# Kernel optimization log

Hardware: AMD Instinct MI355X
Metric: run time of the kernel (lower is better)

The kernel has to match this reference:

```python
import jax, jax.numpy as jnp
import numpy as np

H, W = 80, 80
LOWPASS = 0.3   # 3DGS low-pass filter added to 2D covariance diagonal
NEAR = 0.2      # near-plane cull depth


def quat_to_rot(q):
    # q: [N,4] (w,x,y,z) -> [N,3,3]
    w, x, y, z = q[..., 0], q[..., 1], q[..., 2], q[..., 3]
    return jnp.stack([
        jnp.stack([1 - 2 * (y * y + z * z), 2 * (x * y - w * z), 2 * (x * z + w * y)], -1),
        jnp.stack([2 * (x * y + w * z), 1 - 2 * (x * x + z * z), 2 * (y * z - w * x)], -1),
        jnp.stack([2 * (x * z - w * y), 2 * (y * z + w * x), 1 - 2 * (x * x + y * y)], -1),
    ], -2)


def setup_inputs() -> dict:
    key = jax.random.key(0)
    k1, k2 = jax.random.split(key)
    vsize = 1.25
    def mids(lo, hi, lim):
        g = np.arange(lo, hi + 1e-6, vsize)
        return ((g[:-1] + g[1:]) / 2.0)[:lim]
    xy = mids(-20.0, 20.0, 200)   # 32 midpoints
    zz = mids(-4.0, 4.0, 16)      # 6 midpoints
    X, Y, Z = np.meshgrid(xy, xy, zz, indexing='ij')
    pc_xyz = jnp.asarray(np.stack([X, Y, Z], -1).reshape(-1, 3), jnp.float32)  # [6144,3]
    N = pc_xyz.shape[0]
    B, NC, C = 1, 6, 32
    vox_features = jax.random.normal(k1, (B, N, C), jnp.float32)
    density = jax.random.normal(k2, (B, N), jnp.float32)
    scales = jnp.full((N, 1), float(np.log(vsize)), jnp.float32)
    rots = jnp.concatenate([jnp.ones((N, 1)), jnp.zeros((N, 3))], -1).astype(jnp.float32)
    # 6 surround cameras at origin, yaw = k*60deg; cam axes: x=right, y=up-ish, z=forward
    yaws = np.arange(NC) * (2 * np.pi / NC)
    f = np.stack([np.cos(yaws), np.sin(yaws), np.zeros(NC)], -1)
    r = np.stack([np.sin(yaws), -np.cos(yaws), np.zeros(NC)], -1)
    u = np.cross(f, r)
    Rw2c = np.stack([r, u, f], 1)  # rows are camera axes -> world2cam rotation [NC,3,3]
    cam_rot = jnp.asarray(Rw2c[None], jnp.float32)          # [B,NC,3,3]
    cam_trans = jnp.zeros((B, NC, 3), jnp.float32)          # [B,NC,3]
    cam_intr = jnp.asarray(np.tile(np.array([45.0, 45.0, W / 2.0, H / 2.0], np.float32), (B, NC, 1)))
    return dict(vox_features=vox_features, density=density, cam_rot=cam_rot,
                cam_trans=cam_trans, cam_intr=cam_intr, pc_xyz=pc_xyz,
                scales=scales, rots=rots)


def _render_one(Rcw, t, intr, pc_xyz, Mcov, opacity, feats):
    # Rcw [3,3], t [3], intr [4]; Mcov [N,3,3] = R*diag(s); opacity [N]; feats [N,C]
    fx, fy, cx, cy = intr[0], intr[1], intr[2], intr[3]
    cam = pc_xyz @ Rcw.T + t                    # [N,3] camera-frame means
    tz = jnp.maximum(cam[:, 2], 1e-6)
    valid = (cam[:, 2] > NEAR).astype(pc_xyz.dtype)
    u = fx * cam[:, 0] / tz + cx
    v = fy * cam[:, 1] / tz + cy
    z0 = jnp.zeros_like(tz)
    J = jnp.stack([jnp.stack([fx / tz, z0, -fx * cam[:, 0] / tz ** 2], -1),
                   jnp.stack([z0, fy / tz, -fy * cam[:, 1] / tz ** 2], -1)], -2)  # [N,2,3]
    A = jnp.einsum('nij,jk->nik', J, Rcw)       # J @ W  [N,2,3]
    Bm = jnp.einsum('nij,njk->nik', A, Mcov)    # [N,2,3]
    cov = jnp.einsum('nij,nkj->nik', Bm, Bm)    # 2D covariance [N,2,2]
    a = cov[:, 0, 0] + LOWPASS
    b = cov[:, 0, 1]
    c = cov[:, 1, 1] + LOWPASS
    det = a * c - b * b
    ia, ib, ic = c / det, -b / det, a / det
    # depth-sort (invalid gaussians pushed to the back)
    order = jnp.argsort(tz + (1.0 - valid) * 1e6)
    u, v, ia, ib, ic = u[order], v[order], ia[order], ib[order], ic[order]
    op_s, feat_s, valid_s = opacity[order], feats[order], valid[order]
    px = jnp.arange(W, dtype=pc_xyz.dtype)
    py = jnp.arange(H, dtype=pc_xyz.dtype)
    dx = px[None, None, :] - u[:, None, None]   # [N,1,W] -> broadcast [N,H,W]
    dy = py[None, :, None] - v[:, None, None]   # [N,H,1]
    power = (-0.5 * (ia[:, None, None] * dx * dx + ic[:, None, None] * dy * dy)
             - ib[:, None, None] * dx * dy)
    g = jnp.exp(jnp.minimum(power, 0.0))
    alpha = jnp.clip(op_s[:, None, None] * g, 0.0, 0.99) * valid_s[:, None, None]
    Tcum = jnp.cumprod(1.0 - alpha, axis=0)
    Texc = jnp.concatenate([jnp.ones((1, H, W), alpha.dtype), Tcum[:-1]], 0)  # exclusive transmittance
    return jnp.einsum('nhw,nc->chw', Texc * alpha, feat_s)


def reference(vox_features, density, cam_rot, cam_trans, cam_intr, pc_xyz, scales, rots):
    Bsz, N, C = vox_features.shape
    Rg = quat_to_rot(rots)                      # [N,3,3]
    s = jnp.exp(scales)                         # [N,1] isotropic scale
    Mcov = Rg * s[:, :, None]                   # R @ diag(s,s,s)
    outs = []
    for b in range(Bsz):
        op = jax.nn.softplus(density[b]).reshape(-1)        # opacity activation
        feats = vox_features[b].reshape(-1, C)
        def rone(args):
            R_, t_, K_ = args
            return _render_one(R_, t_, K_, pc_xyz, Mcov, op, feats)
        out_b = jax.lax.map(rone, (cam_rot[b], cam_trans[b], cam_intr[b]))  # [NC,C,H,W]
        outs.append(out_b)
    return jnp.stack(outs)                      # [B,NC,C,H,W]
```

## Files before the change

kernel.cpp:

```cpp
#include <hip/hip_runtime.h>

#define NEARV    0.2f
#define LOWPASSV 0.3f

constexpr int HH = 80, WW = 80;
constexpr int CFE = 32;
constexpr int NZ = 6;

constexpr int NCELL = 1024;
constexpr int HMAX = NCELL * NZ;

typedef unsigned long long u64;
typedef unsigned int u32;

__global__ __launch_bounds__(256) void rank_kernel(
    const float* __restrict__ pc_xyz, const float* __restrict__ cam_rot,
    const float* __restrict__ cam_trans, int N,
    int* __restrict__ counts, int* __restrict__ cellord)
{
  __shared__ u32 sk[NCELL];
  __shared__ u32 wred[4];

  const int cam = blockIdx.y;
  const int tid = threadIdx.x;
  const float* R = cam_rot + cam*9;
  const float R20 = R[6], R21 = R[7], R22 = R[8];
  const float t2  = cam_trans[cam*3+2];

  int vcnt = 0;
  #pragma unroll
  for (int e4 = 0; e4 < NCELL/256; ++e4) {
    const int cell = e4*256 + tid;
    const int i0 = cell * NZ;
    u32 key22 = 0x3FFFFFu;
    if (i0 < N) {
      float c2 = R20*pc_xyz[i0*3+0] + R21*pc_xyz[i0*3+1] + R22*pc_xyz[i0*3+2] + t2;
      if (c2 > NEARV) {
        u32 b = __float_as_uint(c2) - 0x3E000000u;
        b = b < 0x03FFFF00u ? b : 0x03FFFF00u;
        key22 = b >> 4;
        ++vcnt;
      }
    }
    sk[cell] = (key22 << 10) | (u32)cell;
  }
  __syncthreads();

  const int e = blockIdx.x * 256 + tid;
  const u32 mykey = sk[e];
  const uint4* k4 = (const uint4*)sk;
  int rank = 0;
  #pragma unroll 8
  for (int i = 0; i < NCELL/4; ++i) {
    const uint4 kv = k4[i];
    rank += (int)(kv.x < mykey) + (int)(kv.y < mykey)
          + (int)(kv.z < mykey) + (int)(kv.w < mykey);
  }

  cellord[(size_t)cam * NCELL + rank] = e;

  if (blockIdx.x == 0) {
    #pragma unroll
    for (int off = 32; off > 0; off >>= 1) vcnt += __shfl_down(vcnt, off, 64);
    if ((tid & 63) == 0) wred[tid >> 6] = (u32)vcnt;
    __syncthreads();
    if (tid == 0)
      counts[cam] = (int)(wred[0] + wred[1] + wred[2] + wred[3]) * NZ;
  }
}

__global__ __launch_bounds__(256) void proj_kernel(
    const float* __restrict__ pc_xyz, const float* __restrict__ cam_rot,
    const float* __restrict__ cam_trans, const float* __restrict__ cam_intr,
    const float* __restrict__ density, const float* __restrict__ scales,
    int N, int NC,
    const int* __restrict__ counts, const int* __restrict__ cellord,
    float4* __restrict__ hdrA, float4* __restrict__ hdrB)
{
  const int cam = blockIdx.y;
  const int kq = blockIdx.x * 256 + threadIdx.x;
  if (kq >= counts[cam]) return;

  const int cellp = kq / NZ;
  const int n = cellord[(size_t)cam * NCELL + cellp] * NZ + (kq - cellp * NZ);

  const float* R = cam_rot + cam*9;
  const float* t = cam_trans + cam*3;
  const float* intr = cam_intr + cam*4;
  const float fx = intr[0], fy = intr[1], cx = intr[2], cy = intr[3];
  const int b = cam / NC;

  const float p0 = pc_xyz[n*3+0], p1 = pc_xyz[n*3+1], p2 = pc_xyz[n*3+2];
  const float c0 = R[0]*p0 + R[1]*p1 + R[2]*p2 + t[0];
  const float c1 = R[3]*p0 + R[4]*p1 + R[5]*p2 + t[1];
  const float c2 = R[6]*p0 + R[7]*p1 + R[8]*p2 + t[2];
  const float tz = fmaxf(c2, 1e-6f);
  const float itz = 1.0f / tz;
  const float u = fx*c0*itz + cx;
  const float v = fy*c1*itz + cy;
  const float j00 = fx*itz, j02 = -(fx*c0*itz)*itz;
  const float j11 = fy*itz, j12 = -(fy*c1*itz)*itz;
  const float s = expf(scales[n]);
  const float s2 = s*s;
  const float cov00 = s2*(j00*j00 + j02*j02);
  const float cov01 = s2*(j02*j12);
  const float cov11 = s2*(j11*j11 + j12*j12);
  const float a = cov00 + LOWPASSV, bb = cov01, cc = cov11 + LOWPASSV;
  const float det = a*cc - bb*bb;
  const float idet = 1.0f / det;
  const float mid = 0.5f*(a + cc);
  const float dd = sqrtf(fmaxf(mid*mid - det, 0.f));
  float r2 = 32.f * (mid + dd);
  const float dens = density[(size_t)b*N + n];
  const float op = fmaxf(dens, 0.f) + log1pf(expf(-fabsf(dens)));
  const float sx = fminf(fmaxf(u, 0.f), (float)(WW-1)) - u;
  const float sy = fminf(fmaxf(v, 0.f), (float)(HH-1)) - v;
  if (sx*sx + sy*sy > r2) r2 = -1.0f;

  hdrA[(size_t)cam * HMAX + kq] = make_float4(u, v, cc*idet, -bb*idet);
  hdrB[(size_t)cam * HMAX + kq] = make_float4(a*idet, op, r2, __int_as_float(n));
}

__global__ __launch_bounds__(64) void render_kernel(
    const float* __restrict__ vox,
    const float4* __restrict__ hdrA, const float4* __restrict__ hdrB,
    const int* __restrict__ counts,
    float* __restrict__ out, int N, int NC)
{
  __shared__ float4 cA[64], cB[64];
  __shared__ int   cgi[64];
  __shared__ float4 sfeat[64];

  const int cam = blockIdx.y;
  const int tile = blockIdx.x;
  const int tx = tile % (WW/8), ty = tile / (WW/8);
  const int lane = threadIdx.x;
  const int p  = lane & 31;
  const int h  = lane >> 5;
  const int lx = p & 7, ly = p >> 3;
  const int px = tx*8 + lx, py = ty*4 + ly;
  const float fpx = (float)px, fpy = (float)py;
  const float tx0 = (float)(tx*8), tx1 = tx0 + 7.f;
  const float ty0 = (float)(ty*4), ty1 = ty0 + 3.f;
  const int count = counts[cam];
  const int b = cam / NC;
  const float4* hA = hdrA + (size_t)cam * HMAX;
  const float4* hB = hdrB + (size_t)cam * HMAX;
  const float4* voxb = (const float4*)vox + (size_t)b * N * (CFE/4);

  float acc[CFE/2];
  #pragma unroll
  for (int i = 0; i < CFE/2; ++i) acc[i] = 0.f;
  float T = 1.0f;
  bool done = false;

  if (count > 0) {
    const int kcf = min(lane, count - 1);
    float4 na = hA[kcf], nb = hB[kcf];

    for (int k0 = 0; k0 < count && !done; k0 += 64) {
      const float4 a0 = na, b0 = nb;
      if (k0 + 64 < count) {
        const int kn = min(k0 + 64 + lane, count - 1);
        na = hA[kn]; nb = hB[kn];
      }
      const int ki = k0 + lane;
      const float ddx = fminf(fmaxf(a0.x, tx0), tx1) - a0.x;
      const float ddy = fminf(fmaxf(a0.y, ty0), ty1) - a0.y;
      const bool hit = (ki < count) && (ddx*ddx + ddy*ddy <= b0.z);
      const u64 m = __ballot(hit);
      const int P = __popcll(m);
      if (P == 0) continue;
      __syncthreads();
      if (hit) {
        const int pos = (int)__popcll(m & ((1ull << lane) - 1ull));
        cA[pos] = a0;
        cB[pos] = b0;
        cgi[pos] = __float_as_int(b0.w);
      }
      __syncthreads();

      const int sl = lane >> 3, sc = lane & 7;
      float4 pf = voxb[(size_t)cgi[min(sl, P - 1)] * (CFE/4) + sc];

      for (int j = 0; j < P; j += 8) {
        sfeat[lane] = pf;
        if (j + 8 < P) {
          const int si = min(j + 8 + sl, P - 1);
          pf = voxb[(size_t)cgi[si] * (CFE/4) + sc];
        }
        __syncthreads();

        float al[8];
        #pragma unroll
        for (int qq = 0; qq < 8; ++qq) {
          const int idx = j + qq;
          const float4 a1 = cA[idx & 63];
          const float4 a2 = cB[idx & 63];
          const float dx = fpx - a1.x, dy = fpy - a1.y;
          const float power = -0.5f*(a1.z*dx*dx + a2.x*dy*dy) - a1.w*dx*dy;
          float av = fminf(a2.y * __expf(fminf(power, 0.f)), 0.99f);
          av = (power > -16.f) ? av : 0.f;
          al[qq] = (idx < P) ? av : 0.f;
        }
        #pragma unroll
        for (int qq = 0; qq < 8; ++qq) {
          const float w = T * al[qq];
          T -= w;
          if (__any(w > 1e-8f)) {
            const float4* fj = &sfeat[qq * 8 + 4 * h];
            #pragma unroll
            for (int c4 = 0; c4 < 4; ++c4) {
              const float4 fv = fj[c4];
              acc[c4*4+0] += w*fv.x; acc[c4*4+1] += w*fv.y;
              acc[c4*4+2] += w*fv.z; acc[c4*4+3] += w*fv.w;
            }
          }
        }
        if (__all(T < 1e-3f)) { done = true; break; }
        __syncthreads();
      }
    }
  }
  float* ob = out + (((size_t)cam * CFE + 16*h) * HH + py) * WW + px;
  #pragma unroll
  for (int c = 0; c < CFE/2; ++c) ob[(size_t)c * HH * WW] = acc[c];
}

extern "C" void kernel_launch(void* const* d_in, const int* in_sizes, int n_in,
                              void* d_out, int out_size, void* d_ws, size_t ws_size,
                              hipStream_t stream) {
  const float* vox       = (const float*)d_in[0];
  const float* density   = (const float*)d_in[1];
  const float* cam_rot   = (const float*)d_in[2];
  const float* cam_trans = (const float*)d_in[3];
  const float* cam_intr  = (const float*)d_in[4];
  const float* pc_xyz    = (const float*)d_in[5];
  const float* scales    = (const float*)d_in[6];
  float* out = (float*)d_out;

  const int N    = in_sizes[5] / 3;
  const int NCAM = in_sizes[4] / 4;
  const int B    = in_sizes[1] / N;
  const int NC   = NCAM / B;

  unsigned char* ws = (unsigned char*)d_ws;
  int* countsPtr = (int*)ws;
  int* cellord   = (int*)(ws + 256);
  float4* hdrA   = (float4*)(ws + 32768);
  float4* hdrB   = (float4*)(ws + 32768 + (size_t)NCAM * HMAX * sizeof(float4));

  rank_kernel<<<dim3(NCELL/256, NCAM), 256, 0, stream>>>(
      pc_xyz, cam_rot, cam_trans, N, countsPtr, cellord);
  proj_kernel<<<dim3((HMAX + 255) / 256, NCAM), 256, 0, stream>>>(
      pc_xyz, cam_rot, cam_trans, cam_intr, density, scales, N, NC,
      countsPtr, cellord, hdrA, hdrB);
  render_kernel<<<dim3((WW/8)*(HH/4), NCAM), 64, 0, stream>>>(
      vox, hdrA, hdrB, countsPtr, out, N, NC);
}
```

Before: 85.12 us.

## Prefetch splat headers four chunks ahead and split rank comparisons across thread pairs

```diff
diff --git a/kernel.cpp b/kernel.cpp
--- a/kernel.cpp
+++ b/kernel.cpp
@@ -13,13 +13,13 @@
 typedef unsigned long long u64;
 typedef unsigned int u32;
 
-__global__ __launch_bounds__(256) void rank_kernel(
+__global__ __launch_bounds__(512) void rank_kernel(
     const float* __restrict__ pc_xyz, const float* __restrict__ cam_rot,
     const float* __restrict__ cam_trans, int N,
     int* __restrict__ counts, int* __restrict__ cellord)
 {
   __shared__ u32 sk[NCELL];
-  __shared__ u32 wred[4];
+  __shared__ u32 wred[8];
 
   const int cam = blockIdx.y;
   const int tid = threadIdx.x;
@@ -29,8 +29,8 @@
 
   int vcnt = 0;
   #pragma unroll
-  for (int e4 = 0; e4 < NCELL/256; ++e4) {
-    const int cell = e4*256 + tid;
+  for (int e2 = 0; e2 < NCELL/512; ++e2) {
+    const int cell = e2*512 + tid;
     const int i0 = cell * NZ;
     u32 key22 = 0x3FFFFFu;
     if (i0 < N) {
@@ -46,26 +46,33 @@
   }
   __syncthreads();
 
-  const int e = blockIdx.x * 256 + tid;
-  const u32 mykey = sk[e];
+  const int cell = blockIdx.x * 256 + (tid >> 1);
+  const u32 mykey = sk[cell];
   const uint4* k4 = (const uint4*)sk;
+  const int h0 = (tid & 1) * (NCELL/8);
   int rank = 0;
   #pragma unroll 8
-  for (int i = 0; i < NCELL/4; ++i) {
-    const uint4 kv = k4[i];
+  for (int i = 0; i < NCELL/8; ++i) {
+    const uint4 kv = k4[h0 + i];
     rank += (int)(kv.x < mykey) + (int)(kv.y < mykey)
           + (int)(kv.z < mykey) + (int)(kv.w < mykey);
   }
-
-  cellord[(size_t)cam * NCELL + rank] = e;
+  rank += __shfl_xor(rank, 1, 64);
+
+  if ((tid & 1) == 0)
+    cellord[(size_t)cam * NCELL + rank] = cell;
 
   if (blockIdx.x == 0) {
     #pragma unroll
     for (int off = 32; off > 0; off >>= 1) vcnt += __shfl_down(vcnt, off, 64);
     if ((tid & 63) == 0) wred[tid >> 6] = (u32)vcnt;
     __syncthreads();
-    if (tid == 0)
-      counts[cam] = (int)(wred[0] + wred[1] + wred[2] + wred[3]) * NZ;
+    if (tid == 0) {
+      u32 tot = 0;
+      #pragma unroll
+      for (int w = 0; w < 8; ++w) tot += wred[w];
+      counts[cam] = (int)tot * NZ;
+    }
   }
 }
 
@@ -154,74 +161,96 @@
   float T = 1.0f;
   bool done = false;
 
+#define LOAD4(Aarr, Barr, base_) do {                                   \
+    _Pragma("unroll")                                                   \
+    for (int d_ = 0; d_ < 4; ++d_) {                                    \
+      const int kn_ = min((base_) + d_*64 + lane, count - 1);           \
+      Aarr[d_] = hA[kn_]; Barr[d_] = hB[kn_];                           \
+    } } while (0)
+
+#define PROCESS_CHUNK(k0_, a0_, b0_) do {                               \
+    const int ki = (k0_) + lane;                                        \
+    const float ddx = fminf(fmaxf((a0_).x, tx0), tx1) - (a0_).x;        \
+    const float ddy = fminf(fmaxf((a0_).y, ty0), ty1) - (a0_).y;        \
+    const bool hit = (ki < count) && (ddx*ddx + ddy*ddy <= (b0_).z);    \
+    const u64 m = __ballot(hit);                                        \
+    const int P = __popcll(m);                                          \
+    if (P == 0) continue;                                               \
+    __syncthreads();                   \
+    if (hit) {                                                          \
+      const int pos = (int)__popcll(m & ((1ull << lane) - 1ull));       \
+      cA[pos] = (a0_); cB[pos] = (b0_);                                 \
+      cgi[pos] = __float_as_int((b0_).w);                               \
+    }                                                                   \
+    __syncthreads();                                                    \
+    const int sl = lane >> 3, sc = lane & 7;                            \
+    float4 pf = voxb[(size_t)cgi[min(sl, P - 1)] * (CFE/4) + sc];       \
+    for (int j = 0; j < P; j += 8) {                                    \
+      sfeat[lane] = pf;                                                 \
+      if (j + 8 < P) {                                                  \
+        const int si = min(j + 8 + sl, P - 1);                          \
+        pf = voxb[(size_t)cgi[si] * (CFE/4) + sc];                      \
+      }                                                                 \
+      __syncthreads();                                                  \
+      float al[8];                                                      \
+      _Pragma("unroll")                                                 \
+      for (int qq = 0; qq < 8; ++qq) {                                  \
+        const int idx = j + qq;                                         \
+        const float4 a1 = cA[idx & 63];                                 \
+        const float4 a2 = cB[idx & 63];                                 \
+        const float dx = fpx - a1.x, dy = fpy - a1.y;                   \
+        const float power = -0.5f*(a1.z*dx*dx + a2.x*dy*dy) - a1.w*dx*dy; \
+        float av = fminf(a2.y * __expf(fminf(power, 0.f)), 0.99f);      \
+        av = (power > -16.f) ? av : 0.f;                                \
+        al[qq] = (idx < P) ? av : 0.f;                                  \
+      }                                                                 \
+      _Pragma("unroll")                                                 \
+      for (int qq = 0; qq < 8; ++qq) {                                  \
+        const float w = T * al[qq];                                     \
+        T -= w;                                                         \
+        if (__any(w > 1e-8f)) {                                         \
+          const float4* fj = &sfeat[qq * 8 + 4 * h];                    \
+          _Pragma("unroll")                                             \
+          for (int c4 = 0; c4 < 4; ++c4) {                              \
+            const float4 fv = fj[c4];                                   \
+            acc[c4*4+0] += w*fv.x; acc[c4*4+1] += w*fv.y;               \
+            acc[c4*4+2] += w*fv.z; acc[c4*4+3] += w*fv.w;               \
+          }                                                             \
+        }                                                               \
+      }                                                                 \
+      if (__all(T < 1e-3f)) { done = true; break; }                     \
+      __syncthreads();                                                  \
+    }                                                                   \
+  } while (0)
+
   if (count > 0) {
-    const int kcf = min(lane, count - 1);
-    float4 na = hA[kcf], nb = hB[kcf];
-
-    for (int k0 = 0; k0 < count && !done; k0 += 64) {
-      const float4 a0 = na, b0 = nb;
-      if (k0 + 64 < count) {
-        const int kn = min(k0 + 64 + lane, count - 1);
-        na = hA[kn]; nb = hB[kn];
+    float4 A0x[4], B0x[4], A1x[4], B1x[4];
+    const int nquad = (count + 255) >> 8;
+    LOAD4(A0x, B0x, 0);
+
+    for (int q = 0; q < nquad && !done; q += 2) {
+      if (q + 1 < nquad) LOAD4(A1x, B1x, (q+1)*256);
+      #pragma unroll
+      for (int d = 0; d < 4; ++d) {
+        if (done) break;
+        const int k0 = q*256 + d*64;
+        if (k0 >= count) break;
+        PROCESS_CHUNK(k0, A0x[d], B0x[d]);
       }
-      const int ki = k0 + lane;
-      const float ddx = fminf(fmaxf(a0.x, tx0), tx1) - a0.x;
-      const float ddy = fminf(fmaxf(a0.y, ty0), ty1) - a0.y;
-      const bool hit = (ki < count) && (ddx*ddx + ddy*ddy <= b0.z);
-      const u64 m = __ballot(hit);
-      const int P = __popcll(m);
-      if (P == 0) continue;
-      __syncthreads();
-      if (hit) {
-        const int pos = (int)__popcll(m & ((1ull << lane) - 1ull));
-        cA[pos] = a0;
-        cB[pos] = b0;
-        cgi[pos] = __float_as_int(b0.w);
-      }
-      __syncthreads();
-
-      const int sl = lane >> 3, sc = lane & 7;
-      float4 pf = voxb[(size_t)cgi[min(sl, P - 1)] * (CFE/4) + sc];
-
-      for (int j = 0; j < P; j += 8) {
-        sfeat[lane] = pf;
-        if (j + 8 < P) {
-          const int si = min(j + 8 + sl, P - 1);
-          pf = voxb[(size_t)cgi[si] * (CFE/4) + sc];
-        }
-        __syncthreads();
-
-        float al[8];
-        #pragma unroll
-        for (int qq = 0; qq < 8; ++qq) {
-          const int idx = j + qq;
-          const float4 a1 = cA[idx & 63];
-          const float4 a2 = cB[idx & 63];
-          const float dx = fpx - a1.x, dy = fpy - a1.y;
-          const float power = -0.5f*(a1.z*dx*dx + a2.x*dy*dy) - a1.w*dx*dy;
-          float av = fminf(a2.y * __expf(fminf(power, 0.f)), 0.99f);
-          av = (power > -16.f) ? av : 0.f;
-          al[qq] = (idx < P) ? av : 0.f;
-        }
-        #pragma unroll
-        for (int qq = 0; qq < 8; ++qq) {
-          const float w = T * al[qq];
-          T -= w;
-          if (__any(w > 1e-8f)) {
-            const float4* fj = &sfeat[qq * 8 + 4 * h];
-            #pragma unroll
-            for (int c4 = 0; c4 < 4; ++c4) {
-              const float4 fv = fj[c4];
-              acc[c4*4+0] += w*fv.x; acc[c4*4+1] += w*fv.y;
-              acc[c4*4+2] += w*fv.z; acc[c4*4+3] += w*fv.w;
-            }
-          }
-        }
-        if (__all(T < 1e-3f)) { done = true; break; }
-        __syncthreads();
+      if (done || q + 1 >= nquad) break;
+      if (q + 2 < nquad) LOAD4(A0x, B0x, (q+2)*256);
+      #pragma unroll
+      for (int d = 0; d < 4; ++d) {
+        if (done) break;
+        const int k0 = (q+1)*256 + d*64;
+        if (k0 >= count) break;
+        PROCESS_CHUNK(k0, A1x[d], B1x[d]);
       }
     }
   }
+#undef PROCESS_CHUNK
+#undef LOAD4
+
   float* ob = out + (((size_t)cam * CFE + 16*h) * HH + py) * WW + px;
   #pragma unroll
   for (int c = 0; c < CFE/2; ++c) ob[(size_t)c * HH * WW] = acc[c];
@@ -250,7 +279,7 @@
   float4* hdrA   = (float4*)(ws + 32768);
   float4* hdrB   = (float4*)(ws + 32768 + (size_t)NCAM * HMAX * sizeof(float4));
 
-  rank_kernel<<<dim3(NCELL/256, NCAM), 256, 0, stream>>>(
+  rank_kernel<<<dim3(NCELL/256, NCAM), 512, 0, stream>>>(
       pc_xyz, cam_rot, cam_trans, N, countsPtr, cellord);
   proj_kernel<<<dim3((HMAX + 255) / 256, NCAM), 256, 0, stream>>>(
       pc_xyz, cam_rot, cam_trans, cam_intr, density, scales, N, NC,
```

Measured after the change: 83.14 us. 2.3% less time.
